# Kernel tuning notes

Measured on AMD Instinct MI355X. Metric: run time of the kernel, lower is better.

Reference implementation:

```python
import jax, jax.numpy as jnp
import numpy as np

N_NODES = 100000


def _gcn_conv(x, W, b, src, dst, num_nodes):
    # PyG GCNConv: h = x @ W, symmetric norm deg^{-1/2} (self-loops already in src/dst),
    # out[i] = sum_{j->i} norm_ij * h[j] + b
    h = x @ W
    deg = jax.ops.segment_sum(jnp.ones_like(src, dtype=x.dtype), dst, num_segments=num_nodes)
    dinv = jnp.where(deg > 0, jax.lax.rsqrt(jnp.maximum(deg, 1.0)), 0.0)
    norm = dinv[src] * dinv[dst]  # [E]
    msg = h[src] * norm[:, None]  # gather + scale, [E, d]
    out = jax.ops.segment_sum(msg, dst, num_segments=num_nodes)
    return out + b


def setup_inputs() -> dict:
    key = jax.random.key(0)
    k1, k2, k3, k4 = jax.random.split(key, 4)
    d = 64
    E = 1600000
    x = jax.random.normal(k1, (N_NODES, d), dtype=jnp.float32)
    edge_index = jax.random.randint(k2, (2, E), 0, N_NODES, dtype=jnp.int64)
    W1 = jax.random.normal(k3, (d, d), dtype=jnp.float32) / np.sqrt(d)
    b1 = jnp.zeros((d,), dtype=jnp.float32)
    W2 = jax.random.normal(k4, (d, d), dtype=jnp.float32) / np.sqrt(d)
    b2 = jnp.zeros((d,), dtype=jnp.float32)
    return {"x": x, "edge_index": edge_index, "W1": W1, "b1": b1, "W2": W2, "b2": b2}


def reference(x, edge_index, W1, b1, W2, b2):
    num_nodes = x.shape[0]
    # add self loops once (shared by both convs)
    loops = jnp.arange(num_nodes, dtype=edge_index.dtype)
    src = jnp.concatenate([edge_index[0], loops])
    dst = jnp.concatenate([edge_index[1], loops])
    x1 = jax.nn.relu(_gcn_conv(x, W1, b1, src, dst, num_nodes))
    # dropout in eval mode == identity (deterministic reference)
    x2 = _gcn_conv(x1, W2, b2, src, dst, num_nodes)
    return x2 + x
```

## Files before the change

### kernel.cpp

```cpp
#include <hip/hip_runtime.h>
#include <hip/hip_bf16.h>

#define DFEAT 64
#define BNODES 128
#define BCAP 2560
#define EPB 2048

typedef __attribute__((ext_vector_type(8))) short short8;
typedef __attribute__((ext_vector_type(4))) float f32x4;

__device__ __forceinline__ unsigned short f2bf(float f) {
    unsigned u = __float_as_uint(f);
    return (unsigned short)((u + 0x7FFFu + ((u >> 16) & 1u)) >> 16);
}
__device__ __forceinline__ float bflo(unsigned u) { return __uint_as_float(u << 16); }
__device__ __forceinline__ float bfhi(unsigned u) { return __uint_as_float(u & 0xFFFF0000u); }


__global__ __launch_bounds__(256) void zero_cur_k(int* __restrict__ bcur, int n) {
    int i = blockIdx.x * 256 + threadIdx.x;
    if (i < n) bcur[i] = 0;
}

__global__ __launch_bounds__(256) void bucketize_k(const int* __restrict__ src,
                                                   const int* __restrict__ dst,
                                                   int* __restrict__ bcur,
                                                   unsigned* __restrict__ barr,
                                                   int E, int NB) {
    __shared__ unsigned pkbuf[EPB];
    __shared__ unsigned short bbuf[EPB];
    __shared__ int hist[784];
    __shared__ int base[784];

    int tid = threadIdx.x;
    int e0 = blockIdx.x * EPB;
    int n = min(EPB, E - e0);

    for (int t = tid; t < NB; t += 256) hist[t] = 0;
    __syncthreads();

    for (int k = 0; k < EPB / 256; ++k) {
        int i = k * 256 + tid;
        if (i < n) {
            int d = dst[e0 + i];
            int b = d >> 7;
            pkbuf[i] = ((unsigned)(d & 127) << 25) | (unsigned)src[e0 + i];
            bbuf[i] = (unsigned short)b;
            atomicAdd(&hist[b], 1);
        }
    }
    __syncthreads();

    for (int t = tid; t < NB; t += 256) {
        int c = hist[t];
        if (c > 0) base[t] = atomicAdd(&bcur[t], c);
        hist[t] = 0;
    }
    __syncthreads();

    for (int k = 0; k < EPB / 256; ++k) {
        int i = k * 256 + tid;
        if (i < n) {
            int b = bbuf[i];
            int loc = atomicAdd(&hist[b], 1);
            int pos = base[b] + loc;
            if (pos < BCAP) barr[(size_t)b * BCAP + pos] = pkbuf[i];
        }
    }
}

__global__ __launch_bounds__(256) void localsort_k(const int* __restrict__ bcur,
                                                   unsigned* __restrict__ barr,
                                                   int* __restrict__ meta,
                                                   float* __restrict__ dinv, int N) {
    __shared__ int cnt[BNODES];
    __shared__ int off[BNODES];
    __shared__ int cur[BNODES];
    __shared__ int sorted[BCAP];
    int b = blockIdx.x;
    int nb = min(bcur[b], BCAP);
    const unsigned* p = barr + (size_t)b * BCAP;
    if (threadIdx.x < BNODES) cnt[threadIdx.x] = 0;
    __syncthreads();
    for (int i = threadIdx.x; i < nb; i += 256) atomicAdd(&cnt[p[i] >> 25], 1);
    __syncthreads();
    if (threadIdx.x < BNODES) off[threadIdx.x] = cnt[threadIdx.x];
    __syncthreads();
    for (int d = 1; d < BNODES; d <<= 1) {
        int v = 0;
        if (threadIdx.x < BNODES && threadIdx.x >= d) v = off[threadIdx.x - d];
        __syncthreads();
        if (threadIdx.x < BNODES) off[threadIdx.x] += v;
        __syncthreads();
    }
    if (threadIdx.x < BNODES) {
        int ex = off[threadIdx.x] - cnt[threadIdx.x];
        cur[threadIdx.x] = ex;
        int node = b * BNODES + threadIdx.x;
        if (node < N) {
            meta[node] = (ex << 16) | cnt[threadIdx.x];
            dinv[node] = rsqrtf((float)cnt[threadIdx.x] + 1.0f);
        }
    }
    __syncthreads();
    for (int i = threadIdx.x; i < nb; i += 256) {
        unsigned w = p[i];
        int pos = atomicAdd(&cur[w >> 25], 1);
        sorted[pos] = (int)(w & 0x1FFFFFFu);
    }
    __syncthreads();
    int tot = off[BNODES - 1];
    for (int i = threadIdx.x; i < tot; i += 256)
        barr[(size_t)b * BCAP + i] = (unsigned)sorted[i];
}


__global__ __launch_bounds__(256) void prepW_k(const float* __restrict__ W1,
                                               const float* __restrict__ W2,
                                               unsigned short* __restrict__ W1f,
                                               unsigned short* __restrict__ W2f) {
    for (int idx = threadIdx.x; idx < 4096; idx += 256) {
        int j = idx & 7, lane = (idx >> 3) & 63, ct = (idx >> 9) & 3, kb = (idx >> 11) & 1;
        int k = kb * 32 + (lane >> 4) * 8 + j;
        int col = ct * 16 + (lane & 15);
        W1f[idx] = f2bf(W1[k * 64 + col]);
        W2f[idx] = f2bf(W2[k * 64 + col]);
    }
}


template <bool F32IN>
__global__ __launch_bounds__(256) void mgemm_k(const void* __restrict__ Xin,
                                               const unsigned short* __restrict__ Wf,
                                               const float* __restrict__ dinv,
                                               unsigned short* __restrict__ Ab,
                                               int ntile, int N) {
    int wv = threadIdx.x >> 6, l = threadIdx.x & 63;
    int tile = blockIdx.x * 4 + wv;
    if (tile >= ntile) return;
    int row0 = tile * 16;
    int ar = row0 + (l & 15);

    short8 a0, a1;
    if constexpr (F32IN) {
        const float* Xf = (const float*)Xin;
        const float4* q = (const float4*)(Xf + (size_t)ar * 64 + (l >> 4) * 8);
        float4 f0 = q[0], f1 = q[1];
        const float4* q2 = (const float4*)(Xf + (size_t)ar * 64 + 32 + (l >> 4) * 8);
        float4 g0 = q2[0], g1 = q2[1];
        a0[0]=(short)f2bf(f0.x); a0[1]=(short)f2bf(f0.y); a0[2]=(short)f2bf(f0.z); a0[3]=(short)f2bf(f0.w);
        a0[4]=(short)f2bf(f1.x); a0[5]=(short)f2bf(f1.y); a0[6]=(short)f2bf(f1.z); a0[7]=(short)f2bf(f1.w);
        a1[0]=(short)f2bf(g0.x); a1[1]=(short)f2bf(g0.y); a1[2]=(short)f2bf(g0.z); a1[3]=(short)f2bf(g0.w);
        a1[4]=(short)f2bf(g1.x); a1[5]=(short)f2bf(g1.y); a1[6]=(short)f2bf(g1.z); a1[7]=(short)f2bf(g1.w);
    } else {
        const short8* Xv = (const short8*)Xin;
        a0 = Xv[ar * 8 + (l >> 4)];
        a1 = Xv[ar * 8 + 4 + (l >> 4)];
    }

    const short8* Wv = (const short8*)Wf;
    int rbase = row0 + (l >> 4) * 4;
    float dv0 = dinv[rbase + 0], dv1 = dinv[rbase + 1];
    float dv2 = dinv[rbase + 2], dv3 = dinv[rbase + 3];

#pragma unroll
    for (int ct = 0; ct < 4; ++ct) {
        f32x4 c = {0.0f, 0.0f, 0.0f, 0.0f};
        c = __builtin_amdgcn_mfma_f32_16x16x32_bf16(a0, Wv[ct * 64 + l], c, 0, 0, 0);
        c = __builtin_amdgcn_mfma_f32_16x16x32_bf16(a1, Wv[(4 + ct) * 64 + l], c, 0, 0, 0);
        int colb = ct * 16 + (l & 15);
        Ab[(size_t)(rbase + 0) * 64 + colb] = f2bf(c[0] * dv0);
        Ab[(size_t)(rbase + 1) * 64 + colb] = f2bf(c[1] * dv1);
        Ab[(size_t)(rbase + 2) * 64 + colb] = f2bf(c[2] * dv2);
        Ab[(size_t)(rbase + 3) * 64 + colb] = f2bf(c[3] * dv3);
    }
}


#define GATHER_BODY(...)                                                            \
    int tid = threadIdx.x;                                                          \
    int lane = tid & 31;                                                            \
    int g = lane >> 3;                                         \
    int sl = lane & 7;                                         \
    int node = blockIdx.x * 8 + (tid >> 5);                                         \
    if (node >= N) return;                                                          \
    int m = meta[node];                                                             \
    int cnt = m & 0xFFFF;                                                           \
    const int* lst = (const int*)ed + (size_t)(node >> 7) * BCAP + (m >> 16);       \
    const uint4* A4 = (const uint4*)Au;                                             \
    float a0 = 0, a1 = 0, a2 = 0, a3 = 0, a4 = 0, a5 = 0, a6 = 0, a7 = 0;           \
    if (g == 0) {                                                    \
        uint4 su = A4[(size_t)node * 8 + sl];                                       \
        a0 = bflo(su.x); a1 = bfhi(su.x); a2 = bflo(su.y); a3 = bfhi(su.y);         \
        a4 = bflo(su.z); a5 = bfhi(su.z); a6 = bflo(su.w); a7 = bfhi(su.w);         \
    }                                                                               \
    int i = 0;                                                                      \
    for (; i + 8 <= cnt; i += 8) {                                                  \
        int sA = lst[i + g];                                                        \
        int sB = lst[i + 4 + g];                                                    \
        uint4 uA = A4[(size_t)sA * 8 + sl];                                         \
        uint4 uB = A4[(size_t)sB * 8 + sl];                                         \
        a0 += bflo(uA.x) + bflo(uB.x); a1 += bfhi(uA.x) + bfhi(uB.x);               \
        a2 += bflo(uA.y) + bflo(uB.y); a3 += bfhi(uA.y) + bfhi(uB.y);               \
        a4 += bflo(uA.z) + bflo(uB.z); a5 += bfhi(uA.z) + bfhi(uB.z);               \
        a6 += bflo(uA.w) + bflo(uB.w); a7 += bfhi(uA.w) + bfhi(uB.w);               \
    }                                                                               \
    for (; i < cnt; i += 4) {                                                       \
        int e = min(i + g, cnt - 1);                                                \
        int s = lst[e];                                                             \
        uint4 u = A4[(size_t)s * 8 + sl];                                           \
        if (i + g >= cnt) { u.x = 0; u.y = 0; u.z = 0; u.w = 0; }                   \
        a0 += bflo(u.x); a1 += bfhi(u.x); a2 += bflo(u.y); a3 += bfhi(u.y);         \
        a4 += bflo(u.z); a5 += bfhi(u.z); a6 += bflo(u.w); a7 += bfhi(u.w);         \
    }                                                                               \
    a0 += __shfl_xor(a0, 8);  a1 += __shfl_xor(a1, 8);                              \
    a2 += __shfl_xor(a2, 8);  a3 += __shfl_xor(a3, 8);                              \
    a4 += __shfl_xor(a4, 8);  a5 += __shfl_xor(a5, 8);                              \
    a6 += __shfl_xor(a6, 8);  a7 += __shfl_xor(a7, 8);                              \
    a0 += __shfl_xor(a0, 16); a1 += __shfl_xor(a1, 16);                             \
    a2 += __shfl_xor(a2, 16); a3 += __shfl_xor(a3, 16);                             \
    a4 += __shfl_xor(a4, 16); a5 += __shfl_xor(a5, 16);                             \
    a6 += __shfl_xor(a6, 16); a7 += __shfl_xor(a7, 16);                             \
    if (g == 0) {                                                                   \
        float d = dinv[node];                                                       \
        float4 b0 = *(const float4*)(bias + sl * 8);                                \
        float4 b1 = *(const float4*)(bias + sl * 8 + 4);                            \
        __VA_ARGS__                                                                 \
    }

__global__ __launch_bounds__(256) void gat_relu_k(const int* __restrict__ meta,
                                                  const unsigned* __restrict__ ed,
                                                  const unsigned short* __restrict__ Au,
                                                  const float* __restrict__ dinv,
                                                  const float* __restrict__ bias,
                                                  unsigned* __restrict__ xout, int N) {
    GATHER_BODY(
        float r0 = fmaxf(fmaf(d, a0, b0.x), 0.0f);
        float r1 = fmaxf(fmaf(d, a1, b0.y), 0.0f);
        float r2 = fmaxf(fmaf(d, a2, b0.z), 0.0f);
        float r3 = fmaxf(fmaf(d, a3, b0.w), 0.0f);
        float r4 = fmaxf(fmaf(d, a4, b1.x), 0.0f);
        float r5 = fmaxf(fmaf(d, a5, b1.y), 0.0f);
        float r6 = fmaxf(fmaf(d, a6, b1.z), 0.0f);
        float r7 = fmaxf(fmaf(d, a7, b1.w), 0.0f);
        uint4 pk;
        pk.x = ((unsigned)f2bf(r1) << 16) | f2bf(r0);
        pk.y = ((unsigned)f2bf(r3) << 16) | f2bf(r2);
        pk.z = ((unsigned)f2bf(r5) << 16) | f2bf(r4);
        pk.w = ((unsigned)f2bf(r7) << 16) | f2bf(r6);
        ((uint4*)xout)[(size_t)node * 8 + sl] = pk;
    )
}

__global__ __launch_bounds__(256) void gat_res_k(const int* __restrict__ meta,
                                                 const unsigned* __restrict__ ed,
                                                 const unsigned short* __restrict__ Au,
                                                 const float* __restrict__ dinv,
                                                 const float* __restrict__ bias,
                                                 const float* __restrict__ xres,
                                                 float* __restrict__ out, int N) {
    GATHER_BODY(
        const float4* xq = (const float4*)(xres + (size_t)node * 64 + sl * 8);
        float4 x0 = xq[0];
        float4 x1 = xq[1];
        float4 r0;
        float4 r1;
        r0.x = fmaf(d, a0, b0.x + x0.x); r0.y = fmaf(d, a1, b0.y + x0.y);
        r0.z = fmaf(d, a2, b0.z + x0.z); r0.w = fmaf(d, a3, b0.w + x0.w);
        r1.x = fmaf(d, a4, b1.x + x1.x); r1.y = fmaf(d, a5, b1.y + x1.y);
        r1.z = fmaf(d, a6, b1.z + x1.z); r1.w = fmaf(d, a7, b1.w + x1.w);
        float4* oq = (float4*)(out + (size_t)node * 64 + sl * 8);
        oq[0] = r0; oq[1] = r1;
    )
}


extern "C" void kernel_launch(void* const* d_in, const int* in_sizes, int n_in,
                              void* d_out, int out_size, void* d_ws, size_t ws_size,
                              hipStream_t stream) {
    const float* x = (const float*)d_in[0];
    const int* ei = (const int*)d_in[1];
    const float* W1 = (const float*)d_in[2];
    const float* b1 = (const float*)d_in[3];
    const float* W2 = (const float*)d_in[4];
    const float* b2 = (const float*)d_in[5];
    float* out = (float*)d_out;

    const int N = in_sizes[0] / DFEAT;
    const int E = in_sizes[1] / 2;
    const int NB = (N + BNODES - 1) / BNODES;
    const int NT = (N + 15) / 16;

    const int* src = ei;
    const int* dst = ei + E;

    char* w = (char*)d_ws;
    size_t o = 0;
    unsigned short* Xb = (unsigned short*)(w + o); o += (size_t)N * DFEAT * 2;
    unsigned short* Ab = (unsigned short*)(w + o); o += (size_t)N * DFEAT * 2;
    float* dinv = (float*)(w + o);                 o += ((size_t)N * 4 + 255) & ~255;
    int* meta = (int*)(w + o);                     o += ((size_t)N * 4 + 255) & ~255;
    int* bcur = (int*)(w + o);                     o += ((size_t)NB * 4 + 255) & ~255;
    unsigned short* W1f = (unsigned short*)(w + o); o += 4096 * 2;
    unsigned short* W2f = (unsigned short*)(w + o); o += 4096 * 2;
    o = (o + 255) & ~255;
    unsigned* barr = (unsigned*)(w + o);

    const int gB = (E + EPB - 1) / EPB;
    const int gG = (N + 7) / 8;
    const int gM = (NT + 3) / 4;

    zero_cur_k<<<(NB + 255) / 256, 256, 0, stream>>>(bcur, NB);
    bucketize_k<<<gB, 256, 0, stream>>>(src, dst, bcur, barr, E, NB);
    localsort_k<<<NB, 256, 0, stream>>>(bcur, barr, meta, dinv, N);
    prepW_k<<<1, 256, 0, stream>>>(W1, W2, W1f, W2f);

    mgemm_k<true><<<gM, 256, 0, stream>>>(x, W1f, dinv, Ab, NT, N);
    gat_relu_k<<<gG, 256, 0, stream>>>(meta, barr, Ab, dinv, b1, (unsigned*)Xb, N);

    mgemm_k<false><<<gM, 256, 0, stream>>>(Xb, W2f, dinv, Ab, NT, N);
    gat_res_k<<<gG, 256, 0, stream>>>(meta, barr, Ab, dinv, b2, x, out, N);
}
```

Baseline: 149.2 us.

## Split features into two column planes and gather each plane separately

Stores the intermediate node features as two planes of 32 columns each and launches each gather kernel with twice the blocks, so each block processes one plane of its nodes. This halves the footprint of the randomly gathered table per pass, aiming for better cache hit rates on the irregular neighbour reads. The cost is reading the edge lists and metadata twice, with more reduction shuffles. The weight-preparation kernel is folded into an extra block of the local-sort launch to save a launch.

```diff
diff --git a/kernel.cpp b/kernel.cpp
--- a/kernel.cpp
+++ b/kernel.cpp
@@ -72,12 +72,27 @@
 __global__ __launch_bounds__(256) void localsort_k(const int* __restrict__ bcur,
                                                    unsigned* __restrict__ barr,
                                                    int* __restrict__ meta,
-                                                   float* __restrict__ dinv, int N) {
+                                                   float* __restrict__ dinv, int N,
+                                                   const float* __restrict__ W1,
+                                                   const float* __restrict__ W2,
+                                                   unsigned short* __restrict__ W1f,
+                                                   unsigned short* __restrict__ W2f,
+                                                   int NB) {
+    int b = blockIdx.x;
+    if (b >= NB) {
+        for (int idx = threadIdx.x; idx < 4096; idx += 256) {
+            int j = idx & 7, lane = (idx >> 3) & 63, ct = (idx >> 9) & 3, kb = (idx >> 11) & 1;
+            int k = kb * 32 + (lane >> 4) * 8 + j;
+            int col = ct * 16 + (lane & 15);
+            W1f[idx] = f2bf(W1[k * 64 + col]);
+            W2f[idx] = f2bf(W2[k * 64 + col]);
+        }
+        return;
+    }
     __shared__ int cnt[BNODES];
     __shared__ int off[BNODES];
     __shared__ int cur[BNODES];
     __shared__ int sorted[BCAP];
-    int b = blockIdx.x;
     int nb = min(bcur[b], BCAP);
     const unsigned* p = barr + (size_t)b * BCAP;
     if (threadIdx.x < BNODES) cnt[threadIdx.x] = 0;
@@ -112,20 +127,6 @@
     int tot = off[BNODES - 1];
     for (int i = threadIdx.x; i < tot; i += 256)
         barr[(size_t)b * BCAP + i] = (unsigned)sorted[i];
-}
-
-
-__global__ __launch_bounds__(256) void prepW_k(const float* __restrict__ W1,
-                                               const float* __restrict__ W2,
-                                               unsigned short* __restrict__ W1f,
-                                               unsigned short* __restrict__ W2f) {
-    for (int idx = threadIdx.x; idx < 4096; idx += 256) {
-        int j = idx & 7, lane = (idx >> 3) & 63, ct = (idx >> 9) & 3, kb = (idx >> 11) & 1;
-        int k = kb * 32 + (lane >> 4) * 8 + j;
-        int col = ct * 16 + (lane & 15);
-        W1f[idx] = f2bf(W1[k * 64 + col]);
-        W2f[idx] = f2bf(W2[k * 64 + col]);
-    }
 }
 
 
@@ -153,9 +154,10 @@
         a1[0]=(short)f2bf(g0.x); a1[1]=(short)f2bf(g0.y); a1[2]=(short)f2bf(g0.z); a1[3]=(short)f2bf(g0.w);
         a1[4]=(short)f2bf(g1.x); a1[5]=(short)f2bf(g1.y); a1[6]=(short)f2bf(g1.z); a1[7]=(short)f2bf(g1.w);
     } else {
-        const short8* Xv = (const short8*)Xin;
-        a0 = Xv[ar * 8 + (l >> 4)];
-        a1 = Xv[ar * 8 + 4 + (l >> 4)];
+        const short8* P0 = (const short8*)Xin;
+        const short8* P1 = P0 + (size_t)N * 4;
+        a0 = P0[(size_t)ar * 4 + (l >> 4)];
+        a1 = P1[(size_t)ar * 4 + (l >> 4)];
     }
 
     const short8* Wv = (const short8*)Wf;
@@ -169,10 +171,12 @@
         c = __builtin_amdgcn_mfma_f32_16x16x32_bf16(a0, Wv[ct * 64 + l], c, 0, 0, 0);
         c = __builtin_amdgcn_mfma_f32_16x16x32_bf16(a1, Wv[(4 + ct) * 64 + l], c, 0, 0, 0);
         int colb = ct * 16 + (l & 15);
-        Ab[(size_t)(rbase + 0) * 64 + colb] = f2bf(c[0] * dv0);
-        Ab[(size_t)(rbase + 1) * 64 + colb] = f2bf(c[1] * dv1);
-        Ab[(size_t)(rbase + 2) * 64 + colb] = f2bf(c[2] * dv2);
-        Ab[(size_t)(rbase + 3) * 64 + colb] = f2bf(c[3] * dv3);
+        unsigned short* plane = Ab + (size_t)(colb >> 5) * N * 32;
+        int within = colb & 31;
+        plane[(size_t)(rbase + 0) * 32 + within] = f2bf(c[0] * dv0);
+        plane[(size_t)(rbase + 1) * 32 + within] = f2bf(c[1] * dv1);
+        plane[(size_t)(rbase + 2) * 32 + within] = f2bf(c[2] * dv2);
+        plane[(size_t)(rbase + 3) * 32 + within] = f2bf(c[3] * dv3);
     }
 }
 
@@ -180,39 +184,50 @@
 #define GATHER_BODY(...)                                                            \
     int tid = threadIdx.x;                                                          \
     int lane = tid & 31;                                                            \
-    int g = lane >> 3;                                         \
-    int sl = lane & 7;                                         \
-    int node = blockIdx.x * 8 + (tid >> 5);                                         \
+    int g = lane >> 2;                                         \
+    int sl2 = lane & 3;                               \
+    int half = (blockIdx.x >= (unsigned)nBlk) ? 1 : 0;                              \
+    int node = (blockIdx.x - half * nBlk) * 8 + (tid >> 5);                         \
     if (node >= N) return;                                                          \
     int m = meta[node];                                                             \
     int cnt = m & 0xFFFF;                                                           \
     const int* lst = (const int*)ed + (size_t)(node >> 7) * BCAP + (m >> 16);       \
-    const uint4* A4 = (const uint4*)Au;                                             \
+    const uint4* A4 = (const uint4*)(Au + (size_t)half * N * 32);   \
     float a0 = 0, a1 = 0, a2 = 0, a3 = 0, a4 = 0, a5 = 0, a6 = 0, a7 = 0;           \
     if (g == 0) {                                                    \
-        uint4 su = A4[(size_t)node * 8 + sl];                                       \
+        uint4 su = A4[(size_t)node * 4 + sl2];                                      \
         a0 = bflo(su.x); a1 = bfhi(su.x); a2 = bflo(su.y); a3 = bfhi(su.y);         \
         a4 = bflo(su.z); a5 = bfhi(su.z); a6 = bflo(su.w); a7 = bfhi(su.w);         \
     }                                                                               \
     int i = 0;                                                                      \
+    for (; i + 16 <= cnt; i += 16) {                                                \
+        int s0 = lst[i + g];                                                        \
+        int s1 = lst[i + 8 + g];                                                    \
+        uint4 u0 = A4[(size_t)s0 * 4 + sl2];                                        \
+        uint4 u1 = A4[(size_t)s1 * 4 + sl2];                                        \
+        a0 += bflo(u0.x) + bflo(u1.x); a1 += bfhi(u0.x) + bfhi(u1.x);               \
+        a2 += bflo(u0.y) + bflo(u1.y); a3 += bfhi(u0.y) + bfhi(u1.y);               \
+        a4 += bflo(u0.z) + bflo(u1.z); a5 += bfhi(u0.z) + bfhi(u1.z);               \
+        a6 += bflo(u0.w) + bflo(u1.w); a7 += bfhi(u0.w) + bfhi(u1.w);               \
+    }                                                                               \
     for (; i + 8 <= cnt; i += 8) {                                                  \
-        int sA = lst[i + g];                                                        \
-        int sB = lst[i + 4 + g];                                                    \
-        uint4 uA = A4[(size_t)sA * 8 + sl];                                         \
-        uint4 uB = A4[(size_t)sB * 8 + sl];                                         \
-        a0 += bflo(uA.x) + bflo(uB.x); a1 += bfhi(uA.x) + bfhi(uB.x);               \
-        a2 += bflo(uA.y) + bflo(uB.y); a3 += bfhi(uA.y) + bfhi(uB.y);               \
-        a4 += bflo(uA.z) + bflo(uB.z); a5 += bfhi(uA.z) + bfhi(uB.z);               \
-        a6 += bflo(uA.w) + bflo(uB.w); a7 += bfhi(uA.w) + bfhi(uB.w);               \
+        int s = lst[i + g];                                                         \
+        uint4 u = A4[(size_t)s * 4 + sl2];                                          \
+        a0 += bflo(u.x); a1 += bfhi(u.x); a2 += bflo(u.y); a3 += bfhi(u.y);         \
+        a4 += bflo(u.z); a5 += bfhi(u.z); a6 += bflo(u.w); a7 += bfhi(u.w);         \
     }                                                                               \
-    for (; i < cnt; i += 4) {                                                       \
+    for (; i < cnt; i += 8) {                                                       \
         int e = min(i + g, cnt - 1);                                                \
         int s = lst[e];                                                             \
-        uint4 u = A4[(size_t)s * 8 + sl];                                           \
+        uint4 u = A4[(size_t)s * 4 + sl2];                                          \
         if (i + g >= cnt) { u.x = 0; u.y = 0; u.z = 0; u.w = 0; }                   \
         a0 += bflo(u.x); a1 += bfhi(u.x); a2 += bflo(u.y); a3 += bfhi(u.y);         \
         a4 += bflo(u.z); a5 += bfhi(u.z); a6 += bflo(u.w); a7 += bfhi(u.w);         \
     }                                                                               \
+    a0 += __shfl_xor(a0, 4);  a1 += __shfl_xor(a1, 4);                              \
+    a2 += __shfl_xor(a2, 4);  a3 += __shfl_xor(a3, 4);                              \
+    a4 += __shfl_xor(a4, 4);  a5 += __shfl_xor(a5, 4);                              \
+    a6 += __shfl_xor(a6, 4);  a7 += __shfl_xor(a7, 4);                              \
     a0 += __shfl_xor(a0, 8);  a1 += __shfl_xor(a1, 8);                              \
     a2 += __shfl_xor(a2, 8);  a3 += __shfl_xor(a3, 8);                              \
     a4 += __shfl_xor(a4, 8);  a5 += __shfl_xor(a5, 8);                              \
@@ -222,9 +237,10 @@
     a4 += __shfl_xor(a4, 16); a5 += __shfl_xor(a5, 16);                             \
     a6 += __shfl_xor(a6, 16); a7 += __shfl_xor(a7, 16);                             \
     if (g == 0) {                                                                   \
+        int slot = half * 4 + sl2;               \
         float d = dinv[node];                                                       \
-        float4 b0 = *(const float4*)(bias + sl * 8);                                \
-        float4 b1 = *(const float4*)(bias + sl * 8 + 4);                            \
+        float4 b0 = *(const float4*)(bias + slot * 8);                              \
+        float4 b1 = *(const float4*)(bias + slot * 8 + 4);                          \
         __VA_ARGS__                                                                 \
     }
 
@@ -233,7 +249,8 @@
                                                   const unsigned short* __restrict__ Au,
                                                   const float* __restrict__ dinv,
                                                   const float* __restrict__ bias,
-                                                  unsigned* __restrict__ xout, int N) {
+                                                  unsigned short* __restrict__ xout,
+                                                  int N, int nBlk) {
     GATHER_BODY(
         float r0 = fmaxf(fmaf(d, a0, b0.x), 0.0f);
         float r1 = fmaxf(fmaf(d, a1, b0.y), 0.0f);
@@ -248,7 +265,7 @@
         pk.y = ((unsigned)f2bf(r3) << 16) | f2bf(r2);
         pk.z = ((unsigned)f2bf(r5) << 16) | f2bf(r4);
         pk.w = ((unsigned)f2bf(r7) << 16) | f2bf(r6);
-        ((uint4*)xout)[(size_t)node * 8 + sl] = pk;
+        ((uint4*)(xout + (size_t)half * N * 32))[(size_t)node * 4 + sl2] = pk;
     )
 }
 
@@ -258,9 +275,10 @@
                                                  const float* __restrict__ dinv,
                                                  const float* __restrict__ bias,
                                                  const float* __restrict__ xres,
-                                                 float* __restrict__ out, int N) {
+                                                 float* __restrict__ out,
+                                                 int N, int nBlk) {
     GATHER_BODY(
-        const float4* xq = (const float4*)(xres + (size_t)node * 64 + sl * 8);
+        const float4* xq = (const float4*)(xres + (size_t)node * 64 + slot * 8);
         float4 x0 = xq[0];
         float4 x1 = xq[1];
         float4 r0;
@@ -269,7 +287,7 @@
         r0.z = fmaf(d, a2, b0.z + x0.z); r0.w = fmaf(d, a3, b0.w + x0.w);
         r1.x = fmaf(d, a4, b1.x + x1.x); r1.y = fmaf(d, a5, b1.y + x1.y);
         r1.z = fmaf(d, a6, b1.z + x1.z); r1.w = fmaf(d, a7, b1.w + x1.w);
-        float4* oq = (float4*)(out + (size_t)node * 64 + sl * 8);
+        float4* oq = (float4*)(out + (size_t)node * 64 + slot * 8);
         oq[0] = r0; oq[1] = r1;
     )
 }
@@ -312,12 +330,11 @@
 
     zero_cur_k<<<(NB + 255) / 256, 256, 0, stream>>>(bcur, NB);
     bucketize_k<<<gB, 256, 0, stream>>>(src, dst, bcur, barr, E, NB);
-    localsort_k<<<NB, 256, 0, stream>>>(bcur, barr, meta, dinv, N);
-    prepW_k<<<1, 256, 0, stream>>>(W1, W2, W1f, W2f);
+    localsort_k<<<NB + 1, 256, 0, stream>>>(bcur, barr, meta, dinv, N, W1, W2, W1f, W2f, NB);
 
     mgemm_k<true><<<gM, 256, 0, stream>>>(x, W1f, dinv, Ab, NT, N);
-    gat_relu_k<<<gG, 256, 0, stream>>>(meta, barr, Ab, dinv, b1, (unsigned*)Xb, N);
+    gat_relu_k<<<2 * gG, 256, 0, stream>>>(meta, barr, Ab, dinv, b1, Xb, N, gG);
 
     mgemm_k<false><<<gM, 256, 0, stream>>>(Xb, W2f, dinv, Ab, NT, N);
-    gat_res_k<<<gG, 256, 0, stream>>>(meta, barr, Ab, dinv, b2, x, out, N);
-}
+    gat_res_k<<<2 * gG, 256, 0, stream>>>(meta, barr, Ab, dinv, b2, x, out, N, gG);
+}
```

New measurement: 175.4 us. +17.6%, slower.
